# Optimization experiments

Measured on AMD Instinct MI355X. Metric: run time of the kernel, lower is better.

The kernel has to match this reference:

```python
import jax, jax.numpy as jnp
import numpy as np
from jax import lax

B, C_IN, T = 32, 80, 1000
C = 512          # encoder_embedding_dim
H = C // 2       # LSTM hidden per direction
K = 5            # kernel size
P_ZONEOUT = 0.1
BN_EPS = 1e-5


def setup_inputs() -> dict:
    key = jax.random.key(0)
    ks = jax.random.split(key, 32)
    d = {"x": jax.random.normal(ks[0], (B, C_IN, T), jnp.float32)}
    in_chs = [C_IN, C, C]
    i = 1
    for l in range(3):
        cin = in_chs[l]
        d[f"cw{l}"] = jax.random.normal(ks[i], (C, cin, K), jnp.float32) * (1.0 / np.sqrt(cin * K)); i += 1
        d[f"cb{l}"] = jnp.zeros((C,), jnp.float32)
        d[f"bg{l}"] = jnp.ones((C,), jnp.float32)
        d[f"bb{l}"] = jnp.zeros((C,), jnp.float32)
        d[f"bm{l}"] = jax.random.normal(ks[i], (C,), jnp.float32) * 0.1; i += 1
        d[f"bv{l}"] = jax.random.uniform(ks[i], (C,), jnp.float32, 0.5, 1.5); i += 1
    for tag in ("f", "b"):
        d[f"wih_{tag}"] = jax.random.normal(ks[i], (4 * H, C), jnp.float32) * (1.0 / np.sqrt(C)); i += 1
        d[f"whh_{tag}"] = jax.random.normal(ks[i], (4 * H, H), jnp.float32) * (1.0 / np.sqrt(H)); i += 1
        d[f"bih_{tag}"] = jnp.zeros((4 * H,), jnp.float32)
        d[f"bhh_{tag}"] = jnp.zeros((4 * H,), jnp.float32)
    return d


def _lstm_cell(xt, h, c, wih, whh, bih, bhh):
    g = xt @ wih.T + bih + h @ whh.T + bhh          # [B, 4H]
    i, f, gg, o = jnp.split(g, 4, axis=-1)
    c2 = jax.nn.sigmoid(f) * c + jax.nn.sigmoid(i) * jnp.tanh(gg)
    h2 = jax.nn.sigmoid(o) * jnp.tanh(c2)
    return h2, c2


def _zoneout(old, new, p):
    return p * old + (1.0 - p) * new


def _encoder(x, conv_params, lstm_params):
    # conv + BN(eval) + ReLU stack; dropout is identity in eval mode
    for (cw, cb, bg, bb, bm, bv) in conv_params:
        x = lax.conv_general_dilated(x, cw, (1,), [((K - 1) // 2, (K - 1) // 2)],
                                     dimension_numbers=("NCH", "OIH", "NCH"))
        x = x + cb[None, :, None]
        x = (x - bm[None, :, None]) * (bg / jnp.sqrt(bv + BN_EPS))[None, :, None] + bb[None, :, None]
        x = jax.nn.relu(x)
    x = x.transpose(0, 2, 1)                         # [B, T, C]
    (wih_f, whh_f, bih_f, bhh_f, wih_b, whh_b, bih_b, bhh_b) = lstm_params

    xs_f = x.transpose(1, 0, 2)                      # [T, B, C] forward order
    xs_b = xs_f[::-1]                                # backward order

    def step(carry, inp):
        hf, cf, hb, cb_ = carry
        xf, xb = inp
        hf2, cf2 = _lstm_cell(xf, hf, cf, wih_f, whh_f, bih_f, bhh_f)
        hb2, cb2 = _lstm_cell(xb, hb, cb_, wih_b, whh_b, bih_b, bhh_b)
        hf = _zoneout(hf, hf2, P_ZONEOUT); cf = _zoneout(cf, cf2, P_ZONEOUT)
        hb = _zoneout(hb, hb2, P_ZONEOUT); cb_ = _zoneout(cb_, cb2, P_ZONEOUT)
        return (hf, cf, hb, cb_), (hf, hb)

    z = jnp.zeros((x.shape[0], H), x.dtype)
    _, (out_f, out_b) = lax.scan(step, (z, z, z, z), (xs_f, xs_b))
    out = jnp.concatenate([out_f, out_b[::-1]], axis=-1)  # [T, B, 2H]
    return out.transpose(1, 0, 2)                         # [B, T, 2H]


def reference(x, cw0, cb0, bg0, bb0, bm0, bv0,
              cw1, cb1, bg1, bb1, bm1, bv1,
              cw2, cb2, bg2, bb2, bm2, bv2,
              wih_f, whh_f, bih_f, bhh_f,
              wih_b, whh_b, bih_b, bhh_b):
    conv_params = [(cw0, cb0, bg0, bb0, bm0, bv0),
                   (cw1, cb1, bg1, bb1, bm1, bv1),
                   (cw2, cb2, bg2, bb2, bm2, bv2)]
    lstm_params = (wih_f, whh_f, bih_f, bhh_f, wih_b, whh_b, bih_b, bhh_b)
    return _encoder(x, conv_params, lstm_params)
```

## Files before the change

kernel.cpp:

```cpp
#include <hip/hip_runtime.h>


#define T_LEN 1000
#define NBATCH 32
#define CCH 512
#define HDIM 256
#define GDIM 1024
#define TC 100

typedef _Float16 h16;
typedef _Float16 h16x2 __attribute__((ext_vector_type(2)));
typedef _Float16 f16x8 __attribute__((ext_vector_type(8)));
typedef float    f32x4 __attribute__((ext_vector_type(4)));

__device__ __forceinline__ float fixup(float v, float alt){
    union { float f; unsigned u; } c; c.f = v;
    return ((c.u & 0x7f800000u) == 0x7f800000u) ? alt : v;
}
__device__ __forceinline__ float clamp_s(float v, float lo, float hi){
    return fminf(fmaxf(v, lo), hi);
}
__device__ __forceinline__ float sigm(float x){
    const float xc = clamp_s(x, -30.f, 30.f);
    return 1.0f / (1.0f + __expf(-xc));
}
__device__ __forceinline__ float tanh_safe(float x){
    const float ax = fminf(fabsf(x), 30.0f);
    const float t  = __expf(-2.0f * ax);
    const float r  = (1.0f - t) / (1.0f + t);
    return copysignf(r, x);
}
__device__ __forceinline__ unsigned packh2(float x, float y){
    union Cv { unsigned u; h16 h[2]; };
    Cv c; c.h[0] = (h16)x; c.h[1] = (h16)y;
    return c.u;
}
__device__ __forceinline__ int dot4i8(int a, int b, int c){
#if defined(__has_builtin) && __has_builtin(__builtin_amdgcn_sdot4)
    return __builtin_amdgcn_sdot4(a, b, c, false);
#else
    int r = c;
    #pragma unroll
    for (int k = 0; k < 4; ++k) {
        const int av = (a << (24 - 8*k)) >> 24;
        const int bv = (b << (24 - 8*k)) >> 24;
        r += av * bv;
    }
    return r;
#endif
}

__global__ __launch_bounds__(256)
void pack_convw_kernel(const float* __restrict__ cw, h16* __restrict__ Wp, int cin)
{
    const int n = blockIdx.x*256 + threadIdx.x;
    if (n >= 5*512*cin) return;
    const int k   = n / (512*cin);
    const int rem = n - k*512*cin;
    const int co  = rem / cin;
    const int ci  = rem - co*cin;
    Wp[n] = (h16)cw[((size_t)co*cin + ci)*5 + k];
}

__global__ __launch_bounds__(256)
void pack_wih_kernel(const float* __restrict__ wf, const float* __restrict__ wb, h16* __restrict__ Wg)
{
    const int n = blockIdx.x*256 + threadIdx.x;
    const float* src = (n < 1024*512) ? wf : wb;
    Wg[n] = (h16)src[n & (1024*512 - 1)];
}

__global__ __launch_bounds__(256)
void whh_scale_kernel(const float* __restrict__ whh_f, const float* __restrict__ whh_b,
                      float* __restrict__ scl)
{
    const int n = blockIdx.x*256 + threadIdx.x;
    if (n >= 2048) return;
    const float* whh = (n >= 1024) ? whh_b : whh_f;
    const int row = n & 1023;
    float m = 0.f;
    for (int k = 0; k < HDIM; ++k) m = fmaxf(m, fabsf(whh[(size_t)row*HDIM + k]));
    scl[n] = fmaxf(m, 1e-8f) / 16129.0f;
}

__global__ __launch_bounds__(256)
void whh_prep_kernel(const float* __restrict__ whh_f, const float* __restrict__ whh_b,
                     const float* __restrict__ scl, unsigned* __restrict__ W8)
{
    const int n = blockIdx.x * 256 + threadIdx.x;
    if (n >= 2*16*1024*4) return;
    const int dir   = n >> 16;
    const int rem   = n & 65535;
    const int chunk = rem >> 12;
    const int idx   = rem & 4095;
    const int t     = idx >> 2;
    const int e     = idx & 3;
    const float* whh = dir ? whh_b : whh_f;
    const int half = (t >> 6) & 1;
    const int qq   = t >> 7;
    const int l    = t & 63;
    const int rA   = qq*128 + 2*l;
    int row, g;
    if (chunk < 7)       { row = rA + 1; g = chunk + 1; }
    else if (chunk < 15) { row = rA;     g = chunk - 7; }
    else                 { row = rA + 1; g = 0; }
    const float inv = 1.0f / (scl[dir*1024 + row] * 127.0f);
    const int k0 = 128*half + 16*g + 4*e;
    unsigned u = 0;
    #pragma unroll
    for (int j = 0; j < 4; ++j) {
        const float w = whh[(size_t)row*HDIM + k0 + j];
        int qv = (int)rintf(w * inv);
        qv = qv > 127 ? 127 : (qv < -127 ? -127 : qv);
        u |= ((unsigned)(qv & 0xFF)) << (8*j);
    }
    W8[n] = u;
}

__global__ __launch_bounds__(256)
void x0_transpose_kernel(const float* __restrict__ x, h16* __restrict__ Xt0)
{
    const int b = blockIdx.y;
    const int t = blockIdx.x*256 + threadIdx.x;
    if (t >= T_LEN) return;
    h16 v[80];
    #pragma unroll
    for (int c = 0; c < 80; ++c) v[c] = (h16)x[((size_t)b*80 + c)*T_LEN + t];
    #pragma unroll
    for (int g = 0; g < 10; ++g)
        *(f16x8*)(Xt0 + ((size_t)b*T_LEN + t)*80 + g*8) = *(const f16x8*)(v + g*8);
}

__global__ __attribute__((amdgpu_flat_work_group_size(512,512), amdgpu_waves_per_eu(4,4)))
void conv_mfma_kernel(const h16* __restrict__ Xt, const h16* __restrict__ Wp,
                      h16* __restrict__ outp,
                      const float* __restrict__ cb, const float* __restrict__ bg,
                      const float* __restrict__ bb, const float* __restrict__ bm,
                      const float* __restrict__ bv, int cin)
{
    const int t0   = blockIdx.x * 128;
    const int co0  = blockIdx.y * 128;
    const int b    = blockIdx.z;
    const int tid  = threadIdx.x;
    const int lane = tid & 63;
    const int w    = tid >> 6;
    const int wm   = w >> 2;
    const int wn   = w & 3;
    const int lr   = lane & 15;
    const int lg   = lane >> 4;

    __shared__ __align__(16) h16 Xs[132*40];
    __shared__ __align__(16) h16 Ws[5*128*40];

    f32x4 acc[4][2];
    #pragma unroll
    for (int m = 0; m < 4; ++m)
        #pragma unroll
        for (int n = 0; n < 2; ++n)
            #pragma unroll
            for (int r = 0; r < 4; ++r) acc[m][n][r] = 0.f;

    const int ksteps = (cin + 31) >> 5;
    for (int cs = 0; cs < ksteps; ++cs) {
        const int c0 = cs << 5;
        for (int id = tid; id < 132*4; id += 512) {
            const int row = id >> 2, g = id & 3;
            const int t = t0 + row - 2;
            f16x8 v;
            #pragma unroll
            for (int j = 0; j < 8; ++j) v[j] = (h16)0.f;
            if (t >= 0 && t < T_LEN) {
                const int c = c0 + g*8;
                if (c + 8 <= cin) {
                    v = *(const f16x8*)(Xt + ((size_t)b*T_LEN + t)*cin + c);
                } else if (c < cin) {
                    #pragma unroll
                    for (int j = 0; j < 8; ++j) if (c + j < cin) v[j] = Xt[((size_t)b*T_LEN + t)*cin + c + j];
                }
            }
            *(f16x8*)(Xs + row*40 + g*8) = v;
        }
        for (int id = tid; id < 5*128*4; id += 512) {
            const int k  = id >> 9;
            const int co = (id >> 2) & 127;
            const int g  = id & 3;
            const int c  = c0 + g*8;
            f16x8 v;
            #pragma unroll
            for (int j = 0; j < 8; ++j) v[j] = (h16)0.f;
            if (c + 8 <= cin) {
                v = *(const f16x8*)(Wp + ((size_t)k*512 + co0 + co)*cin + c);
            } else if (c < cin) {
                #pragma unroll
                for (int j = 0; j < 8; ++j) if (c + j < cin) v[j] = Wp[((size_t)k*512 + co0 + co)*cin + c + j];
            }
            *(f16x8*)(Ws + (k*128 + co)*40 + g*8) = v;
        }
        __syncthreads();

        #pragma unroll
        for (int k = 0; k < 5; ++k) {
            const f16x8 b0 = *(const f16x8*)(Ws + (k*128 + wn*32 +      lr)*40 + lg*8);
            const f16x8 b1 = *(const f16x8*)(Ws + (k*128 + wn*32 + 16 + lr)*40 + lg*8);
            #pragma unroll
            for (int m = 0; m < 4; ++m) {
                const f16x8 a = *(const f16x8*)(Xs + (wm*64 + m*16 + lr + k)*40 + lg*8);
                acc[m][0] = __builtin_amdgcn_mfma_f32_16x16x32_f16(a, b0, acc[m][0], 0, 0, 0);
                acc[m][1] = __builtin_amdgcn_mfma_f32_16x16x32_f16(a, b1, acc[m][1], 0, 0, 0);
            }
        }
        __syncthreads();
    }

    #pragma unroll
    for (int nf = 0; nf < 2; ++nf) {
        const int co = co0 + wn*32 + nf*16 + lr;
        const float s  = bg[co] * rsqrtf(fmaxf(bv[co] + 1e-5f, 1e-8f));
        const float sh = (cb[co] - bm[co]) * s + bb[co];
        #pragma unroll
        for (int m = 0; m < 4; ++m) {
            #pragma unroll
            for (int r = 0; r < 4; ++r) {
                const int t = t0 + wm*64 + m*16 + lg*4 + r;
                if (t < T_LEN) {
                    const float y = fixup(clamp_s(fmaxf(acc[m][nf][r]*s + sh, 0.f), 0.f, 60000.f), 0.f);
                    outp[((size_t)b*T_LEN + t)*CCH + co] = (h16)y;
                }
            }
        }
    }
}

__global__ __attribute__((amdgpu_flat_work_group_size(256,256), amdgpu_waves_per_eu(4,4)))
void gates_mfma_kernel(const h16* __restrict__ Xt,
                       const h16* __restrict__ Wg,
                       const float* __restrict__ bih_f, const float* __restrict__ bhh_f,
                       const float* __restrict__ bih_b, const float* __restrict__ bhh_b,
                       h16* __restrict__ G, int t0f, int t0b)
{
    const int tt   = blockIdx.x;
    const int r0   = blockIdx.y * 128;
    const int b    = blockIdx.z & 31;
    const int dir  = blockIdx.z >> 5;
    const int t0c  = dir ? t0b : t0f;
    const int tid  = threadIdx.x;
    const int lane = tid & 63;
    const int w    = tid >> 6;
    const int lr   = lane & 15;
    const int lg   = lane >> 4;
    const float* bi = dir ? bih_b : bih_f;
    const float* bh = dir ? bhh_b : bhh_f;
    const h16* Wd = Wg + (size_t)dir*1024*512;

    __shared__ __align__(16) h16 Xs[64*40];
    __shared__ __align__(16) h16 Ws[128*40];

    f32x4 acc[4][2];
    #pragma unroll
    for (int m = 0; m < 4; ++m)
        #pragma unroll
        for (int n = 0; n < 2; ++n)
            #pragma unroll
            for (int r = 0; r < 4; ++r) acc[m][n][r] = 0.f;

    for (int cs = 0; cs < 16; ++cs) {
        const int c0 = cs << 5;
        for (int id = tid; id < 64*4; id += 256) {
            const int row = id >> 2, g = id & 3;
            int t = t0c + tt*64 + row; if (t >= T_LEN) t = T_LEN - 1;
            *(f16x8*)(Xs + row*40 + g*8) = *(const f16x8*)(Xt + ((size_t)b*T_LEN + t)*CCH + c0 + g*8);
        }
        for (int id = tid; id < 128*4; id += 256) {
            const int row = id >> 2, g = id & 3;
            *(f16x8*)(Ws + row*40 + g*8) = *(const f16x8*)(Wd + (size_t)(r0 + row)*CCH + c0 + g*8);
        }
        __syncthreads();

        const f16x8 b0 = *(const f16x8*)(Ws + (w*32 +      lr)*40 + lg*8);
        const f16x8 b1 = *(const f16x8*)(Ws + (w*32 + 16 + lr)*40 + lg*8);
        #pragma unroll
        for (int m = 0; m < 4; ++m) {
            const f16x8 a = *(const f16x8*)(Xs + (m*16 + lr)*40 + lg*8);
            acc[m][0] = __builtin_amdgcn_mfma_f32_16x16x32_f16(a, b0, acc[m][0], 0, 0, 0);
            acc[m][1] = __builtin_amdgcn_mfma_f32_16x16x32_f16(a, b1, acc[m][1], 0, 0, 0);
        }
        __syncthreads();
    }

    #pragma unroll
    for (int nf = 0; nf < 2; ++nf) {
        const int row = r0 + w*32 + nf*16 + lr;
        const float bias = bi[row] + bh[row];
        #pragma unroll
        for (int m = 0; m < 4; ++m) {
            #pragma unroll
            for (int r = 0; r < 4; ++r) {
                const int tl = tt*64 + m*16 + lg*4 + r;
                if (tl < TC)
                    G[(((size_t)dir*TC + tl)*NBATCH + b)*GDIM + row]
                        = (h16)fixup(clamp_s(acc[m][nf][r] + bias, -60000.f, 60000.f), 0.f);
            }
        }
    }
}

__global__ __attribute__((amdgpu_flat_work_group_size(1024, 1024), amdgpu_waves_per_eu(4, 4)))
void lstm_chunk_kernel(const h16* __restrict__ G,
                       const unsigned* __restrict__ W8,
                       const float* __restrict__ scl,
                       float* __restrict__ state,
                       float* __restrict__ out,
                       int t0f, int t0b, int first)
{
    const int tid  = threadIdx.x;
    const int lane = tid & 63;
    const int half = (tid >> 6) & 1;
    const int q    = tid >> 7;
    const int dir  = blockIdx.x >> 5;
    const int b    = blockIdx.x & 31;
    const int t0   = dir ? t0b : t0f;
    float* st = state + ((size_t)(dir*NBATCH + b))*2*HDIM;
    const uint4* Wg8 = (const uint4*)W8 + (size_t)dir*16384;
    const uint4* Wl8 = Wg8 + 7*1024;

    __shared__ __align__(16) uint4 lw8[9*1024];
    __shared__ __align__(4)  unsigned char hq8[256];
    __shared__ float pbuf[2*GDIM];

    #pragma unroll
    for (int s = 0; s < 9; ++s)
        lw8[s*1024 + tid] = Wl8[s*1024 + tid];

    const int rA = q*128 + 2*lane;
    const float sclA = scl[dir*1024 + rA];
    const float sclB = scl[dir*1024 + rA + 1];

    float hst = 0.0f, cst = 0.0f;
    if (tid < HDIM) {
        if (!first) { hst = st[tid]; cst = st[HDIM + tid]; }
        const int qh = (int)rintf(clamp_s(hst, -1.f, 1.f) * 127.f);
        hq8[tid] = (unsigned char)(qh & 0xFF);
    }
    __syncthreads();

    float2* pbuf2 = (float2*)pbuf;
    float prev_h = 0.0f;
    int   prev_t = -1;

    for (int i = 0; i < TC; ++i) {
        const int sl = dir ? (TC - 1 - i) : i;
        const int t  = t0 + sl;
        const h16* gp = G + (((size_t)dir*TC + sl)*NBATCH + b)*GDIM;

        const unsigned wv = ((const unsigned*)hq8)[(half << 5) | (lane & 31)];

        const uint4 sb0 = Wg8[0*1024 + tid];
        const uint4 sb1 = Wg8[1*1024 + tid];
        const uint4 sb2 = Wg8[2*1024 + tid];
        const uint4 sb3 = Wg8[3*1024 + tid];
        const uint4 sb4 = Wg8[4*1024 + tid];
        const uint4 sb5 = Wg8[5*1024 + tid];
        const uint4 sb6 = Wg8[6*1024 + tid];

        float g0 = 0.f, g1 = 0.f, g2 = 0.f, g3 = 0.f;
        if (tid < HDIM) {
            if (prev_t >= 0)
                out[((size_t)b*T_LEN + prev_t)*(2*HDIM) + dir*HDIM + tid] = prev_h;
            g0 = (float)gp[tid];
            g1 = (float)gp[HDIM + tid];
            g2 = (float)gp[2*HDIM + tid];
            g3 = (float)gp[3*HDIM + tid];
        }

        int s[32];
        #pragma unroll
        for (int j = 0; j < 32; ++j)
            s[j] = __builtin_amdgcn_readlane((int)wv, j);

        int accA = 0, accB = 0;
        #pragma unroll
        for (int g = 0; g < 8; ++g) {
            const uint4 wA = lw8[g*1024 + tid];
            accA = dot4i8(s[4*g + 0], (int)wA.x, accA);
            accA = dot4i8(s[4*g + 1], (int)wA.y, accA);
            accA = dot4i8(s[4*g + 2], (int)wA.z, accA);
            accA = dot4i8(s[4*g + 3], (int)wA.w, accA);
        }
        {
            const uint4 w0 = lw8[8*1024 + tid];
            accB = dot4i8(s[0], (int)w0.x, accB);
            accB = dot4i8(s[1], (int)w0.y, accB);
            accB = dot4i8(s[2], (int)w0.z, accB);
            accB = dot4i8(s[3], (int)w0.w, accB);
        }
        #define ROWB(G_, V_) \
            accB = dot4i8(s[4*(G_) + 0], (int)(V_).x, accB); \
            accB = dot4i8(s[4*(G_) + 1], (int)(V_).y, accB); \
            accB = dot4i8(s[4*(G_) + 2], (int)(V_).z, accB); \
            accB = dot4i8(s[4*(G_) + 3], (int)(V_).w, accB);
        ROWB(1, sb0) ROWB(2, sb1) ROWB(3, sb2) ROWB(4, sb3)
        ROWB(5, sb4) ROWB(6, sb5) ROWB(7, sb6)
        #undef ROWB

        pbuf2[(half << 9) | (q << 6) | lane] = make_float2((float)accA * sclA, (float)accB * sclB);
        __syncthreads();

        if (tid < HDIM) {
            const float gi = g0 + pbuf[tid]            + pbuf[GDIM + tid];
            const float gf = g1 + pbuf[HDIM + tid]     + pbuf[GDIM + HDIM + tid];
            const float gg = g2 + pbuf[2*HDIM + tid]   + pbuf[GDIM + 2*HDIM + tid];
            const float go = g3 + pbuf[3*HDIM + tid]   + pbuf[GDIM + 3*HDIM + tid];
            const float c2 = sigm(gf)*cst + sigm(gi)*tanh_safe(gg);
            const float h2 = sigm(go)*tanh_safe(c2);
            hst = 0.1f*hst + 0.9f*h2;
            cst = 0.1f*cst + 0.9f*c2;
            prev_h = fixup(hst, 50.0f);
            prev_t = t;
            const int qh = (int)rintf(clamp_s(hst, -1.f, 1.f) * 127.f);
            hq8[tid] = (unsigned char)(qh & 0xFF);
        }
        __syncthreads();
    }

    if (tid < HDIM) {
        if (prev_t >= 0)
            out[((size_t)b*T_LEN + prev_t)*(2*HDIM) + dir*HDIM + tid] = prev_h;
        st[tid] = hst; st[HDIM + tid] = cst;
    }
}

extern "C" void kernel_launch(void* const* d_in, const int* in_sizes, int n_in,
                              void* d_out, int out_size, void* d_ws, size_t ws_size,
                              hipStream_t stream)
{
    (void)in_sizes; (void)n_in; (void)out_size;
    if (ws_size < 49152000) return;

    const float* x     = (const float*)d_in[0];
    const float* cw0   = (const float*)d_in[1];
    const float* cb0   = (const float*)d_in[2];
    const float* bg0   = (const float*)d_in[3];
    const float* bb0   = (const float*)d_in[4];
    const float* bm0   = (const float*)d_in[5];
    const float* bv0   = (const float*)d_in[6];
    const float* cw1   = (const float*)d_in[7];
    const float* cb1   = (const float*)d_in[8];
    const float* bg1   = (const float*)d_in[9];
    const float* bb1   = (const float*)d_in[10];
    const float* bm1   = (const float*)d_in[11];
    const float* bv1   = (const float*)d_in[12];
    const float* cw2   = (const float*)d_in[13];
    const float* cb2   = (const float*)d_in[14];
    const float* bg2   = (const float*)d_in[15];
    const float* bb2   = (const float*)d_in[16];
    const float* bm2   = (const float*)d_in[17];
    const float* bv2   = (const float*)d_in[18];
    const float* wih_f = (const float*)d_in[19];
    const float* whh_f = (const float*)d_in[20];
    const float* bih_f = (const float*)d_in[21];
    const float* bhh_f = (const float*)d_in[22];
    const float* wih_b = (const float*)d_in[23];
    const float* whh_b = (const float*)d_in[24];
    const float* bih_b = (const float*)d_in[25];
    const float* bhh_b = (const float*)d_in[26];

    char* ws = (char*)d_ws;
    char* od = (char*)d_out;
    h16*      A   = (h16*)(ws);
    h16*      G   = (h16*)(ws + 32768000);
    float*    st  = (float*)(ws + 45875200);
    unsigned* W8  = (unsigned*)(ws + 46006272);
    float*    scl = (float*)(ws + 46530560);
    h16*      Wg  = (h16*)(ws + 47054848);
    h16*      Bd  = (h16*)(od);
    h16*      Wp0 = (h16*)(od + 36000000);
    h16*      Wp1 = (h16*)(od + 36409600);
    h16*      Wp2 = (h16*)(od + 41652480);
    h16*      Xt0 = (h16*)(od + 46895360);
    float*    out = (float*)d_out;

    pack_convw_kernel<<<dim3((5*512*80  + 255)/256), 256, 0, stream>>>(cw0, Wp0, 80);
    pack_convw_kernel<<<dim3((5*512*512 + 255)/256), 256, 0, stream>>>(cw1, Wp1, 512);
    pack_convw_kernel<<<dim3((5*512*512 + 255)/256), 256, 0, stream>>>(cw2, Wp2, 512);
    pack_wih_kernel<<<dim3(2*1024*512/256), 256, 0, stream>>>(wih_f, wih_b, Wg);
    whh_scale_kernel<<<dim3(8), 256, 0, stream>>>(whh_f, whh_b, scl);
    whh_prep_kernel<<<dim3(512), 256, 0, stream>>>(whh_f, whh_b, scl, W8);
    x0_transpose_kernel<<<dim3(4, 32), 256, 0, stream>>>(x, Xt0);

    const dim3 cgrid(8, 4, 32);
    conv_mfma_kernel<<<cgrid, 512, 0, stream>>>(Xt0, Wp0, A,  cb0, bg0, bb0, bm0, bv0, 80);
    conv_mfma_kernel<<<cgrid, 512, 0, stream>>>(A,   Wp1, Bd, cb1, bg1, bb1, bm1, bv1, 512);
    conv_mfma_kernel<<<cgrid, 512, 0, stream>>>(Bd,  Wp2, A,  cb2, bg2, bb2, bm2, bv2, 512);

    for (int c = 0; c < T_LEN / TC; ++c) {
        const int t0f = c * TC;
        const int t0b = (T_LEN - TC) - c * TC;
        gates_mfma_kernel<<<dim3(2, 8, 64), 256, 0, stream>>>(A, Wg, bih_f, bhh_f, bih_b, bhh_b, G, t0f, t0b);
        lstm_chunk_kernel<<<dim3(64), 1024, 0, stream>>>(G, W8, scl, st, out, t0f, t0b, c == 0);
    }
}
```

Before: 1.770 ms.

## Keep more recurrent weights in registers instead of reloading from global each step

Reorders the int8 recurrent-weight packing so that nine of the sixteen weight slices per thread sit in registers for the whole chunk and the other seven stay in shared memory. Before, seven slices were reloaded from global memory on every timestep. The dot-product loop now reads the hidden-state lanes just in time instead of holding all 32 in an array. This removes per-step global weight traffic and cuts shared-memory use, at the cost of higher register pressure under a fixed waves-per-EU target, which could cause spills.

```diff
diff --git a/kernel.cpp b/kernel.cpp
--- a/kernel.cpp
+++ b/kernel.cpp
@@ -29,11 +29,6 @@
     const float t  = __expf(-2.0f * ax);
     const float r  = (1.0f - t) / (1.0f + t);
     return copysignf(r, x);
-}
-__device__ __forceinline__ unsigned packh2(float x, float y){
-    union Cv { unsigned u; h16 h[2]; };
-    Cv c; c.h[0] = (h16)x; c.h[1] = (h16)y;
-    return c.u;
 }
 __device__ __forceinline__ int dot4i8(int a, int b, int c){
 #if defined(__has_builtin) && __has_builtin(__builtin_amdgcn_sdot4)
@@ -101,9 +96,9 @@
     const int l    = t & 63;
     const int rA   = qq*128 + 2*l;
     int row, g;
-    if (chunk < 7)       { row = rA + 1; g = chunk + 1; }
-    else if (chunk < 15) { row = rA;     g = chunk - 7; }
-    else                 { row = rA + 1; g = 0; }
+    if (chunk < 8)       { row = rA + 1; g = chunk; }
+    else if (chunk == 8) { row = rA;     g = 7; }
+    else                 { row = rA;     g = chunk - 9; }
     const float inv = 1.0f / (scl[dir*1024 + row] * 127.0f);
     const int k0 = 128*half + 16*g + 4*e;
     unsigned u = 0;
@@ -321,15 +316,19 @@
     const int t0   = dir ? t0b : t0f;
     float* st = state + ((size_t)(dir*NBATCH + b))*2*HDIM;
     const uint4* Wg8 = (const uint4*)W8 + (size_t)dir*16384;
-    const uint4* Wl8 = Wg8 + 7*1024;
-
-    __shared__ __align__(16) uint4 lw8[9*1024];
+
+    __shared__ __align__(16) uint4 lw8[7*1024];
     __shared__ __align__(4)  unsigned char hq8[256];
     __shared__ float pbuf[2*GDIM];
 
-    #pragma unroll
-    for (int s = 0; s < 9; ++s)
-        lw8[s*1024 + tid] = Wl8[s*1024 + tid];
+    uint4 rb[8];
+    #pragma unroll
+    for (int g = 0; g < 8; ++g) rb[g] = Wg8[g*1024 + tid];
+    const uint4 ra7 = Wg8[8*1024 + tid];
+
+    #pragma unroll
+    for (int s = 0; s < 7; ++s)
+        lw8[s*1024 + tid] = Wg8[(9 + s)*1024 + tid];
 
     const int rA = q*128 + 2*lane;
     const float sclA = scl[dir*1024 + rA];
@@ -353,14 +352,6 @@
         const h16* gp = G + (((size_t)dir*TC + sl)*NBATCH + b)*GDIM;
 
         const unsigned wv = ((const unsigned*)hq8)[(half << 5) | (lane & 31)];
-
-        const uint4 sb0 = Wg8[0*1024 + tid];
-        const uint4 sb1 = Wg8[1*1024 + tid];
-        const uint4 sb2 = Wg8[2*1024 + tid];
-        const uint4 sb3 = Wg8[3*1024 + tid];
-        const uint4 sb4 = Wg8[4*1024 + tid];
-        const uint4 sb5 = Wg8[5*1024 + tid];
-        const uint4 sb6 = Wg8[6*1024 + tid];
 
         float g0 = 0.f, g1 = 0.f, g2 = 0.f, g3 = 0.f;
         if (tid < HDIM) {
@@ -372,35 +363,24 @@
             g3 = (float)gp[3*HDIM + tid];
         }
 
-        int s[32];
-        #pragma unroll
-        for (int j = 0; j < 32; ++j)
-            s[j] = __builtin_amdgcn_readlane((int)wv, j);
-
         int accA = 0, accB = 0;
         #pragma unroll
         for (int g = 0; g < 8; ++g) {
-            const uint4 wA = lw8[g*1024 + tid];
-            accA = dot4i8(s[4*g + 0], (int)wA.x, accA);
-            accA = dot4i8(s[4*g + 1], (int)wA.y, accA);
-            accA = dot4i8(s[4*g + 2], (int)wA.z, accA);
-            accA = dot4i8(s[4*g + 3], (int)wA.w, accA);
-        }
-        {
-            const uint4 w0 = lw8[8*1024 + tid];
-            accB = dot4i8(s[0], (int)w0.x, accB);
-            accB = dot4i8(s[1], (int)w0.y, accB);
-            accB = dot4i8(s[2], (int)w0.z, accB);
-            accB = dot4i8(s[3], (int)w0.w, accB);
-        }
-        #define ROWB(G_, V_) \
-            accB = dot4i8(s[4*(G_) + 0], (int)(V_).x, accB); \
-            accB = dot4i8(s[4*(G_) + 1], (int)(V_).y, accB); \
-            accB = dot4i8(s[4*(G_) + 2], (int)(V_).z, accB); \
-            accB = dot4i8(s[4*(G_) + 3], (int)(V_).w, accB);
-        ROWB(1, sb0) ROWB(2, sb1) ROWB(3, sb2) ROWB(4, sb3)
-        ROWB(5, sb4) ROWB(6, sb5) ROWB(7, sb6)
-        #undef ROWB
+            const int s0 = __builtin_amdgcn_readlane((int)wv, 4*g + 0);
+            const int s1 = __builtin_amdgcn_readlane((int)wv, 4*g + 1);
+            const int s2 = __builtin_amdgcn_readlane((int)wv, 4*g + 2);
+            const int s3 = __builtin_amdgcn_readlane((int)wv, 4*g + 3);
+            const uint4 wA = (g < 7) ? lw8[g*1024 + tid] : ra7;
+            const uint4 wB = rb[g];
+            accA = dot4i8(s0, (int)wA.x, accA);
+            accA = dot4i8(s1, (int)wA.y, accA);
+            accA = dot4i8(s2, (int)wA.z, accA);
+            accA = dot4i8(s3, (int)wA.w, accA);
+            accB = dot4i8(s0, (int)wB.x, accB);
+            accB = dot4i8(s1, (int)wB.y, accB);
+            accB = dot4i8(s2, (int)wB.z, accB);
+            accB = dot4i8(s3, (int)wB.w, accB);
+        }
 
         pbuf2[(half << 9) | (q << 6) | lane] = make_float2((float)accA * sclA, (float)accB * sclB);
         __syncthreads();
```

New measurement: 1.731 ms. -2.2%, faster.
